# Kernel tuning notes

Measured on AMD Instinct MI355X. Metric: run time of the kernel, lower is better.

The kernel has to match this reference:

```python
import jax, jax.numpy as jnp
import numpy as np

N_POS = 1024
ALPHA = 0.3
B, S = 32, 1024


def setup_inputs() -> dict:
    key = jax.random.key(0)
    k1, k2, k3, k4 = jax.random.split(key, 4)
    s_arc = jax.random.normal(k1, (B, S, S), dtype=jnp.float32)
    a_arc = jax.random.normal(k2, (B, S, S), dtype=jnp.float32)
    adds = jax.random.randint(k3, (B, S), 0, N_POS, dtype=jnp.int32)
    pos = jax.random.randint(k4, (B, S), 0, N_POS, dtype=jnp.int32)
    return {"s_arc": s_arc, "a_arc": a_arc, "adds": adds, "pos": pos}


def reference(s_arc, a_arc, adds, pos):
    n_bins = N_POS * N_POS
    # --- histogram (scatter-add) of a_arc by POS-pair index ---
    # original: _add[b,p1,p2] = adds[b,p1]*seq_len + adds[b,p2]
    sl = adds.shape[1]
    pair_idx = adds[:, :, None] * sl + adds[:, None, :]            # [B,S,S]
    # indices >= n_bins never match any bin in the original masked-sum loop;
    # segment_sum with num_segments=n_bins drops them identically.
    hist = jax.ops.segment_sum(a_arc.reshape(-1), pair_idx.reshape(-1),
                               num_segments=n_bins)                # [n_pos^2]
    score_arc = jax.nn.sigmoid(hist)
    # --- gather score back into s_arc ---
    slp = pos.shape[1]
    pidx = pos[:, :, None] * slp + pos[:, None, :]                  # [B,S,S]
    valid = pidx < n_bins
    gathered = score_arc[jnp.clip(pidx, 0, n_bins - 1)]
    return s_arc + ALPHA * jnp.where(valid, gathered, jnp.float32(0))
```

## Files before the change

kernel.cpp:

```cpp
#include <hip/hip_runtime.h>

#define NPOS 1024
#define BB   32
#define SS   1024
#define ALPHA_C 0.3f
#define OCAP 256
#define MAXO 16
#define PADPAIR 0x10001000u
#define SSTRIDE 1026
#define NZ4 16656
#define NP4 16384

typedef float    __attribute__((ext_vector_type(2))) f32x2;
typedef float    __attribute__((ext_vector_type(4))) f32x4;
typedef int      __attribute__((ext_vector_type(4))) i32x4;
typedef unsigned __attribute__((ext_vector_type(4))) u32x4;

__global__ __launch_bounds__(256) void fill_tables(u32x4* __restrict__ z,
                                                   u32x4* __restrict__ p) {
    const int i = blockIdx.x * 256 + threadIdx.x;
    if (i < NZ4) z[i] = (u32x4){0u, 0u, 0u, 0u};
    else { const int j = i - NZ4; if (j < NP4) p[j] = (u32x4){PADPAIR, PADPAIR, PADPAIR, PADPAIR}; }
}

__global__ __launch_bounds__(256) void build_tables(
    const int* __restrict__ adds, unsigned* __restrict__ rcnt,
    unsigned* __restrict__ scnt, unsigned* __restrict__ bmask,
    ushort* __restrict__ list, ushort* __restrict__ ell16,
    int* __restrict__ ocntc, int* __restrict__ ocntr,
    int* __restrict__ oentc, int* __restrict__ oentr) {
    const int b  = blockIdx.x >> 2;
    const int tg = ((blockIdx.x & 3) << 8) | threadIdx.x;
    const int c  = adds[b * SS + tg];
    const unsigned slot = atomicAdd(&scnt[b * NPOS + c], 1u);
    if (slot < 4u) {
        ell16[(((size_t)b * 512 + (c & 511)) * 2 + (c >> 9)) * 4 + slot] = (ushort)(tg << 2);
    } else {
        const int o = atomicAdd(&ocntc[b], 1);
        if (o < OCAP) oentc[b * OCAP + o] = (c << 10) | tg;
    }
    const unsigned rs = atomicAdd(&rcnt[c * BB + b], 1u);
    if (rs < 4u) {
        list[(size_t)c * 128 + b * 4 + rs] = (ushort)tg;
    } else {
        const int o = atomicAdd(&ocntr[b], 1);
        if (o < OCAP) oentr[b * OCAP + o] = (c << 10) | tg;
        atomicOr(&bmask[b * 32 + (tg >> 5)], 1u << (tg & 31));
    }
}

__global__ __launch_bounds__(512) void hist_rows_kernel(
    const float* __restrict__ a, const unsigned* __restrict__ rcnt,
    const ushort* __restrict__ list, const ushort* __restrict__ ell16,
    float* __restrict__ hist) {
    __shared__ float Sbuf[2][SSTRIDE];
    __shared__ ushort lsrc[128];
    __shared__ int   mcnt_s[32];
    __shared__ ushort actb_s[32];
    __shared__ int   na_s;
    const int r = blockIdx.x, t = threadIdx.x;

    if (t < 128) lsrc[t] = list[(size_t)r * 128 + t];
    if (t < 32)  mcnt_s[t] = min((int)rcnt[r * BB + t], 4);
    if (t < 2)   Sbuf[t][1024] = 0.f;
    __syncthreads();
    if (t == 0) {
        int na = 0;
        for (int b = 0; b < 32; ++b) if (mcnt_s[b]) actb_s[na++] = (ushort)b;
        na_s = na;
    }
    __syncthreads();
    const int na = na_s;
    const u32x4* ellv = (const u32x4*)ell16;
    float acc0 = 0.f, acc1 = 0.f;
    u32x4 E = (u32x4){PADPAIR, PADPAIR, PADPAIR, PADPAIR}, F = E;
    f32x2 R0 = (f32x2){0.f, 0.f}, R1 = R0, R2 = R0, R3 = R0;
    f32x2 T0 = R0, T1 = R0, T2 = R0, T3 = R0;
    int mR = 0, mT = 0;

#define ROWP(bb, s) ((const f32x2*)(a + ((((size_t)(bb) << 10) + lsrc[(bb) * 4 + (s)]) << 10)) + t)

    if (na > 0) {
        const int b0 = actb_s[0], m0 = mcnt_s[b0];
        E = ellv[(size_t)b0 * 512 + t];
        f32x2 S = __builtin_nontemporal_load(ROWP(b0, 0));
        if (m0 > 1) S += __builtin_nontemporal_load(ROWP(b0, 1));
        if (m0 > 2) S += __builtin_nontemporal_load(ROWP(b0, 2));
        if (m0 > 3) S += __builtin_nontemporal_load(ROWP(b0, 3));
        ((f32x2*)&Sbuf[0][0])[t] = S;
        if (na > 1) {
            const int b1 = actb_s[1];
            mR = mcnt_s[b1];
            F = ellv[(size_t)b1 * 512 + t];
            R0 = __builtin_nontemporal_load(ROWP(b1, 0));
            if (mR > 1) R1 = __builtin_nontemporal_load(ROWP(b1, 1));
            if (mR > 2) R2 = __builtin_nontemporal_load(ROWP(b1, 2));
            if (mR > 3) R3 = __builtin_nontemporal_load(ROWP(b1, 3));
        }
        if (na > 2) {
            const int b2 = actb_s[2];
            mT = mcnt_s[b2];
            T0 = __builtin_nontemporal_load(ROWP(b2, 0));
            if (mT > 1) T1 = __builtin_nontemporal_load(ROWP(b2, 1));
            if (mT > 2) T2 = __builtin_nontemporal_load(ROWP(b2, 2));
            if (mT > 3) T3 = __builtin_nontemporal_load(ROWP(b2, 3));
        }
    }
    asm volatile("s_waitcnt lgkmcnt(0)" ::: "memory");
    __builtin_amdgcn_s_barrier();

    for (int j = 0; j < na; ++j) {
        f32x2 U0 = (f32x2){0.f, 0.f}, U1 = U0, U2 = U0, U3 = U0;
        int mU = 0;
        if (j + 3 < na) {
            const int b3 = actb_s[j + 3];
            mU = mcnt_s[b3];
            U0 = __builtin_nontemporal_load(ROWP(b3, 0));
            if (mU > 1) U1 = __builtin_nontemporal_load(ROWP(b3, 1));
            if (mU > 2) U2 = __builtin_nontemporal_load(ROWP(b3, 2));
            if (mU > 3) U3 = __builtin_nontemporal_load(ROWP(b3, 3));
        }
        u32x4 TE = (u32x4){PADPAIR, PADPAIR, PADPAIR, PADPAIR};
        if (j + 2 < na) TE = ellv[(size_t)actb_s[j + 2] * 512 + t];
        if (j + 1 < na) {
            f32x2 S = R0;
            if (mR > 1) S += R1;
            if (mR > 2) S += R2;
            if (mR > 3) S += R3;
            ((f32x2*)&Sbuf[(j + 1) & 1][0])[t] = S;
        }
        const char* rb = (const char*)&Sbuf[j & 1][0];
        acc0 += *(const float*)(rb + (E.x & 0xffffu));
        acc0 += *(const float*)(rb + (E.x >> 16));
        acc0 += *(const float*)(rb + (E.y & 0xffffu));
        acc0 += *(const float*)(rb + (E.y >> 16));
        acc1 += *(const float*)(rb + (E.z & 0xffffu));
        acc1 += *(const float*)(rb + (E.z >> 16));
        acc1 += *(const float*)(rb + (E.w & 0xffffu));
        acc1 += *(const float*)(rb + (E.w >> 16));
        E = F; F = TE;
        R0 = T0; R1 = T1; R2 = T2; R3 = T3; mR = mT;
        T0 = U0; T1 = U1; T2 = U2; T3 = U3; mT = mU;
        __builtin_amdgcn_sched_barrier(0);
        asm volatile("s_waitcnt lgkmcnt(0)" ::: "memory");
        __builtin_amdgcn_s_barrier();
    }
#undef ROWP

    const size_t o0 = (size_t)r * NPOS + t;
    hist[o0]       = acc0;
    hist[o0 + 512] = acc1;
}

__global__ __launch_bounds__(256) void fixup(
    const float* __restrict__ a, const int* __restrict__ adds,
    const int* __restrict__ ocntc, const int* __restrict__ oentc,
    const int* __restrict__ ocntr, const int* __restrict__ oentr,
    const unsigned* __restrict__ bmask, float* __restrict__ hist) {
    const int b = blockIdx.x;
    int y = blockIdx.y;
    if (y < MAXO) {
        if (y >= ocntc[b]) return;
        const int e = oentc[b * OCAP + y];
        const int c = e >> 10, p2 = e & 1023;
        #pragma unroll
        for (int z = 0; z < 4; ++z) {
            const int p = (z << 8) + threadIdx.x;
            if ((bmask[b * 32 + (p >> 5)] >> (p & 31)) & 1u) continue;
            const int r = adds[b * SS + p];
            atomicAdd(&hist[(size_t)r * NPOS + c], a[((size_t)(b * SS + p)) * SS + p2]);
        }
    } else {
        y -= MAXO;
        if (y >= ocntr[b]) return;
        const int e = oentr[b * OCAP + y];
        const int r = e >> 10, p1 = e & 1023;
        #pragma unroll
        for (int z = 0; z < 4; ++z) {
            const int p = (z << 8) + threadIdx.x;
            const int c = adds[b * SS + p];
            atomicAdd(&hist[(size_t)r * NPOS + c], a[((size_t)(b * SS + p1)) * SS + p]);
        }
    }
}

__global__ __launch_bounds__(256) void gather_kernel(
    const float* __restrict__ s, const int* __restrict__ pos,
    const float* __restrict__ score, float* __restrict__ out) {
    __shared__ float srow[NPOS];
    const int row = blockIdx.x;
    const int b   = row >> 10;
    const int*  posb = pos + b * SS;
    const int   base = posb[row & 1023] * NPOS;
    const size_t off = (size_t)row * SS;
    const int t = threadIdx.x;

    const f32x4 sc = ((const f32x4*)(score + base))[t];
    f32x4 v = __builtin_nontemporal_load(((const f32x4*)(s + off)) + t);
    i32x4 c = ((const i32x4*)posb)[t];
    ((f32x4*)srow)[t] = sc;
    __syncthreads();

    const float h0 = srow[c.x], h1 = srow[c.y];
    const float h2 = srow[c.z], h3 = srow[c.w];
    f32x4 o;
    o.x = v.x + ALPHA_C * (1.f / (1.f + __expf(-h0)));
    o.y = v.y + ALPHA_C * (1.f / (1.f + __expf(-h1)));
    o.z = v.z + ALPHA_C * (1.f / (1.f + __expf(-h2)));
    o.w = v.w + ALPHA_C * (1.f / (1.f + __expf(-h3)));
    __builtin_nontemporal_store(o, ((f32x4*)(out + off)) + t);
}

extern "C" void kernel_launch(void* const* d_in, const int* in_sizes, int n_in,
                              void* d_out, int out_size, void* d_ws, size_t ws_size,
                              hipStream_t stream) {
    const float* s_arc = (const float*)d_in[0];
    const float* a_arc = (const float*)d_in[1];
    const int*   adds  = (const int*)d_in[2];
    const int*   pos   = (const int*)d_in[3];
    float* out  = (float*)d_out;

    char* w = (char*)d_ws;
    float*    hist  = (float*)w;                 w += (size_t)NPOS * NPOS * 4;
    unsigned* rcnt  = (unsigned*)w;              w += (size_t)NPOS * BB * 4;
    unsigned* scnt  = (unsigned*)w;              w += (size_t)BB * NPOS * 4;
    unsigned* bmask = (unsigned*)w;              w += (size_t)BB * 32 * 4;
    int*      ocntc = (int*)w;                   w += BB * 4;
    int*      ocntr = (int*)w;                   w += BB * 4;
    ushort*   list  = (ushort*)w;                w += (size_t)NPOS * 128 * 2;
    ushort*   ell16 = (ushort*)w;                w += (size_t)BB * NPOS * 4 * 2;
    int*      oentc = (int*)w;                   w += (size_t)BB * OCAP * 4;
    int*      oentr = (int*)w;

    fill_tables<<<(NZ4 + NP4 + 255) / 256, 256, 0, stream>>>((u32x4*)rcnt, (u32x4*)ell16);
    build_tables<<<4 * BB, 256, 0, stream>>>(adds, rcnt, scnt, bmask, list, ell16,
                                             ocntc, ocntr, oentc, oentr);
    hist_rows_kernel<<<NPOS, 512, 0, stream>>>(a_arc, rcnt, list, ell16, hist);
    fixup<<<dim3(BB, 2 * MAXO), 256, 0, stream>>>(a_arc, adds, ocntc, oentc,
                                                  ocntr, oentr, bmask, hist);
    gather_kernel<<<BB * SS, 256, 0, stream>>>(s_arc, pos, hist, out);
}
```

Baseline: 118.5 us.

## Split hist rows across independent waves with private LDS buffers, removing block barriers

```diff
diff --git a/kernel.cpp b/kernel.cpp
--- a/kernel.cpp
+++ b/kernel.cpp
@@ -7,7 +7,6 @@
 #define OCAP 256
 #define MAXO 16
 #define PADPAIR 0x10001000u
-#define SSTRIDE 1026
 #define NZ4 16656
 #define NP4 16384
 
@@ -49,20 +48,72 @@
     }
 }
 
-__global__ __launch_bounds__(512) void hist_rows_kernel(
+#define HR_BODY(I, RR, EE, MM)                                              \
+  do {                                                                      \
+                  \
+    _Pragma("unroll")                                                       \
+    for (int k = 0; k < 8; ++k) {                                           \
+      f32x2 Sv = RR[0][k];                                                  \
+      if (MM > 1) Sv += RR[1][k];                                           \
+      if (MM > 2) Sv += RR[2][k];                                           \
+      if (MM > 3) Sv += RR[3][k];                                           \
+      ((f32x2*)Sbuf)[l + 64 * k] = Sv;                                      \
+    }                                                                       \
+       \
+    if ((I) + 2 < nah) {                                                    \
+      const int b2_ = actb_s[w + 4 * ((I) + 2)];                            \
+      MM = mcnt_s[b2_];                                                     \
+      _Pragma("unroll")                                                     \
+      for (int s = 0; s < 4; ++s)                                           \
+        if (MM > s) {                                                       \
+          const f32x2* rp_ = (const f32x2*)(a +                             \
+              ((((size_t)b2_ << 10) + lsrc[b2_ * 4 + s]) << 10));           \
+          _Pragma("unroll")                                                 \
+          for (int k = 0; k < 8; ++k)                                       \
+            RR[s][k] = __builtin_nontemporal_load(rp_ + l + 64 * k);        \
+        }                                                                   \
+    } else { MM = 0; }                                                      \
+    __builtin_amdgcn_sched_barrier(0);                                      \
+          \
+    {                                                                       \
+      const char* rb_ = (const char*)Sbuf;                                  \
+      _Pragma("unroll")                                                     \
+      for (int p = 0; p < 8; ++p) {                                         \
+        acc0[p] += *(const float*)(rb_ + (EE[p].x & 0xffffu));              \
+        acc0[p] += *(const float*)(rb_ + (EE[p].x >> 16));                  \
+        acc0[p] += *(const float*)(rb_ + (EE[p].y & 0xffffu));              \
+        acc0[p] += *(const float*)(rb_ + (EE[p].y >> 16));                  \
+        acc1[p] += *(const float*)(rb_ + (EE[p].z & 0xffffu));              \
+        acc1[p] += *(const float*)(rb_ + (EE[p].z >> 16));                  \
+        acc1[p] += *(const float*)(rb_ + (EE[p].w & 0xffffu));              \
+        acc1[p] += *(const float*)(rb_ + (EE[p].w >> 16));                  \
+      }                                                                     \
+    }                                                                       \
+                        \
+    if ((I) + 2 < nah) {                                                    \
+      const int b2e_ = actb_s[w + 4 * ((I) + 2)];                           \
+      _Pragma("unroll")                                                     \
+      for (int p = 0; p < 8; ++p)                                           \
+        EE[p] = ellv[(size_t)b2e_ * 512 + l + 64 * p];                      \
+    }                                                                       \
+  } while (0)
+
+__global__ __launch_bounds__(256, 2) void hist_rows_kernel(
     const float* __restrict__ a, const unsigned* __restrict__ rcnt,
     const ushort* __restrict__ list, const ushort* __restrict__ ell16,
     float* __restrict__ hist) {
-    __shared__ float Sbuf[2][SSTRIDE];
+    __shared__ float Sall[4][1026];
     __shared__ ushort lsrc[128];
-    __shared__ int   mcnt_s[32];
+    __shared__ int mcnt_s[32];
     __shared__ ushort actb_s[32];
-    __shared__ int   na_s;
+    __shared__ int na_s;
     const int r = blockIdx.x, t = threadIdx.x;
+    const int w = t >> 6, l = t & 63;
+    float* Sbuf = &Sall[w][0];
 
     if (t < 128) lsrc[t] = list[(size_t)r * 128 + t];
     if (t < 32)  mcnt_s[t] = min((int)rcnt[r * BB + t], 4);
-    if (t < 2)   Sbuf[t][1024] = 0.f;
+    if (l == 0)  Sall[w][1024] = 0.f;
     __syncthreads();
     if (t == 0) {
         int na = 0;
@@ -70,86 +121,64 @@
         na_s = na;
     }
     __syncthreads();
-    const int na = na_s;
+    const int na  = na_s;
+    const int nah = (na > w) ? ((na - w + 3) >> 2) : 0;
     const u32x4* ellv = (const u32x4*)ell16;
-    float acc0 = 0.f, acc1 = 0.f;
-    u32x4 E = (u32x4){PADPAIR, PADPAIR, PADPAIR, PADPAIR}, F = E;
-    f32x2 R0 = (f32x2){0.f, 0.f}, R1 = R0, R2 = R0, R3 = R0;
-    f32x2 T0 = R0, T1 = R0, T2 = R0, T3 = R0;
-    int mR = 0, mT = 0;
-
-#define ROWP(bb, s) ((const f32x2*)(a + ((((size_t)(bb) << 10) + lsrc[(bb) * 4 + (s)]) << 10)) + t)
-
-    if (na > 0) {
-        const int b0 = actb_s[0], m0 = mcnt_s[b0];
-        E = ellv[(size_t)b0 * 512 + t];
-        f32x2 S = __builtin_nontemporal_load(ROWP(b0, 0));
-        if (m0 > 1) S += __builtin_nontemporal_load(ROWP(b0, 1));
-        if (m0 > 2) S += __builtin_nontemporal_load(ROWP(b0, 2));
-        if (m0 > 3) S += __builtin_nontemporal_load(ROWP(b0, 3));
-        ((f32x2*)&Sbuf[0][0])[t] = S;
-        if (na > 1) {
-            const int b1 = actb_s[1];
-            mR = mcnt_s[b1];
-            F = ellv[(size_t)b1 * 512 + t];
-            R0 = __builtin_nontemporal_load(ROWP(b1, 0));
-            if (mR > 1) R1 = __builtin_nontemporal_load(ROWP(b1, 1));
-            if (mR > 2) R2 = __builtin_nontemporal_load(ROWP(b1, 2));
-            if (mR > 3) R3 = __builtin_nontemporal_load(ROWP(b1, 3));
-        }
-        if (na > 2) {
-            const int b2 = actb_s[2];
-            mT = mcnt_s[b2];
-            T0 = __builtin_nontemporal_load(ROWP(b2, 0));
-            if (mT > 1) T1 = __builtin_nontemporal_load(ROWP(b2, 1));
-            if (mT > 2) T2 = __builtin_nontemporal_load(ROWP(b2, 2));
-            if (mT > 3) T3 = __builtin_nontemporal_load(ROWP(b2, 3));
-        }
-    }
-    asm volatile("s_waitcnt lgkmcnt(0)" ::: "memory");
-    __builtin_amdgcn_s_barrier();
-
-    for (int j = 0; j < na; ++j) {
-        f32x2 U0 = (f32x2){0.f, 0.f}, U1 = U0, U2 = U0, U3 = U0;
-        int mU = 0;
-        if (j + 3 < na) {
-            const int b3 = actb_s[j + 3];
-            mU = mcnt_s[b3];
-            U0 = __builtin_nontemporal_load(ROWP(b3, 0));
-            if (mU > 1) U1 = __builtin_nontemporal_load(ROWP(b3, 1));
-            if (mU > 2) U2 = __builtin_nontemporal_load(ROWP(b3, 2));
-            if (mU > 3) U3 = __builtin_nontemporal_load(ROWP(b3, 3));
-        }
-        u32x4 TE = (u32x4){PADPAIR, PADPAIR, PADPAIR, PADPAIR};
-        if (j + 2 < na) TE = ellv[(size_t)actb_s[j + 2] * 512 + t];
-        if (j + 1 < na) {
-            f32x2 S = R0;
-            if (mR > 1) S += R1;
-            if (mR > 2) S += R2;
-            if (mR > 3) S += R3;
-            ((f32x2*)&Sbuf[(j + 1) & 1][0])[t] = S;
-        }
-        const char* rb = (const char*)&Sbuf[j & 1][0];
-        acc0 += *(const float*)(rb + (E.x & 0xffffu));
-        acc0 += *(const float*)(rb + (E.x >> 16));
-        acc0 += *(const float*)(rb + (E.y & 0xffffu));
-        acc0 += *(const float*)(rb + (E.y >> 16));
-        acc1 += *(const float*)(rb + (E.z & 0xffffu));
-        acc1 += *(const float*)(rb + (E.z >> 16));
-        acc1 += *(const float*)(rb + (E.w & 0xffffu));
-        acc1 += *(const float*)(rb + (E.w >> 16));
-        E = F; F = TE;
-        R0 = T0; R1 = T1; R2 = T2; R3 = T3; mR = mT;
-        T0 = U0; T1 = U1; T2 = U2; T3 = U3; mT = mU;
-        __builtin_amdgcn_sched_barrier(0);
-        asm volatile("s_waitcnt lgkmcnt(0)" ::: "memory");
-        __builtin_amdgcn_s_barrier();
-    }
-#undef ROWP
-
-    const size_t o0 = (size_t)r * NPOS + t;
-    hist[o0]       = acc0;
-    hist[o0 + 512] = acc1;
+
+    float acc0[8], acc1[8];
+    #pragma unroll
+    for (int p = 0; p < 8; ++p) { acc0[p] = 0.f; acc1[p] = 0.f; }
+
+    u32x4 EA[8], EB[8];
+    f32x2 RA[4][8], RB[4][8];
+    int m0v = 0, m1v = 0;
+
+    if (nah > 0) {
+        const int b0 = actb_s[w];
+        m0v = mcnt_s[b0];
+        #pragma unroll
+        for (int p = 0; p < 8; ++p) EA[p] = ellv[(size_t)b0 * 512 + l + 64 * p];
+        #pragma unroll
+        for (int s = 0; s < 4; ++s)
+            if (m0v > s) {
+                const f32x2* rp = (const f32x2*)(a + ((((size_t)b0 << 10) + lsrc[b0 * 4 + s]) << 10));
+                #pragma unroll
+                for (int k = 0; k < 8; ++k) RA[s][k] = __builtin_nontemporal_load(rp + l + 64 * k);
+            }
+    }
+    if (nah > 1) {
+        const int b1 = actb_s[w + 4];
+        m1v = mcnt_s[b1];
+        #pragma unroll
+        for (int p = 0; p < 8; ++p) EB[p] = ellv[(size_t)b1 * 512 + l + 64 * p];
+        #pragma unroll
+        for (int s = 0; s < 4; ++s)
+            if (m1v > s) {
+                const f32x2* rp = (const f32x2*)(a + ((((size_t)b1 << 10) + lsrc[b1 * 4 + s]) << 10));
+                #pragma unroll
+                for (int k = 0; k < 8; ++k) RB[s][k] = __builtin_nontemporal_load(rp + l + 64 * k);
+            }
+    }
+
+    int i = 0;
+    for (; i + 1 < nah; i += 2) {
+        HR_BODY(i,     RA, EA, m0v);
+        HR_BODY(i + 1, RB, EB, m1v);
+    }
+    if (i < nah) HR_BODY(i, RA, EA, m0v);
+
+    #pragma unroll
+    for (int p = 0; p < 8; ++p) {
+        Sbuf[l + 64 * p]       = acc0[p];
+        Sbuf[l + 64 * p + 512] = acc1[p];
+    }
+    __syncthreads();
+    #pragma unroll
+    for (int q = 0; q < 4; ++q) {
+        const int col = (q << 8) + t;
+        hist[(size_t)r * NPOS + col] =
+            Sall[0][col] + Sall[1][col] + Sall[2][col] + Sall[3][col];
+    }
 }
 
 __global__ __launch_bounds__(256) void fixup(
@@ -235,7 +264,7 @@
     fill_tables<<<(NZ4 + NP4 + 255) / 256, 256, 0, stream>>>((u32x4*)rcnt, (u32x4*)ell16);
     build_tables<<<4 * BB, 256, 0, stream>>>(adds, rcnt, scnt, bmask, list, ell16,
                                              ocntc, ocntr, oentc, oentr);
-    hist_rows_kernel<<<NPOS, 512, 0, stream>>>(a_arc, rcnt, list, ell16, hist);
+    hist_rows_kernel<<<NPOS, 256, 0, stream>>>(a_arc, rcnt, list, ell16, hist);
     fixup<<<dim3(BB, 2 * MAXO), 256, 0, stream>>>(a_arc, adds, ocntc, oentc,
                                                   ocntr, oentr, bmask, hist);
     gather_kernel<<<BB * SS, 256, 0, stream>>>(s_arc, pos, hist, out);
```

Result: slower. 218.8 us (+84.7%).
